# Performance work log

Measured on AMD Instinct MI355X. Metric: run time of the kernel, lower is better.

## Reference

```python
import jax, jax.numpy as jnp
import numpy as np

N_NODES = 100000
N_EDGES = 1600000
N_GRAPHS = 512
F_IN, HID, EMB = 256, 64, 2


def gcn_layer(h, src, dst, W, b, n_nodes):
    # PyG GCNConv: h' = D^{-1/2} (A + I) D^{-1/2} (h W) + b
    h = h @ W  # [N, out]
    loop = jnp.arange(n_nodes)
    s = jnp.concatenate([src, loop])
    d = jnp.concatenate([dst, loop])
    deg = jax.ops.segment_sum(jnp.ones_like(d, dtype=h.dtype), d, num_segments=n_nodes)
    dinv = jnp.where(deg > 0, jax.lax.rsqrt(deg), 0.0)
    norm = dinv[s] * dinv[d]  # [E+N]
    msg = h[s] * norm[:, None]  # gather + scale
    return jax.ops.segment_sum(msg, d, num_segments=n_nodes) + b


def setup_inputs() -> dict:
    key = jax.random.key(0)
    k1, k2, k3, k4, k5, k6 = jax.random.split(key, 6)
    x = jax.random.normal(k1, (N_NODES, F_IN), dtype=jnp.float32)
    edge_index = jax.random.randint(k2, (2, N_EDGES), 0, N_NODES, dtype=jnp.int64)
    batch = jnp.sort(jax.random.randint(k3, (N_NODES,), 0, N_GRAPHS, dtype=jnp.int64))
    # Glorot-ish init for layer weights
    W1 = jax.random.normal(k4, (F_IN, HID), dtype=jnp.float32) / np.sqrt(F_IN)
    b1 = jnp.zeros((HID,), dtype=jnp.float32)
    W2 = jax.random.normal(k5, (HID, EMB), dtype=jnp.float32) / np.sqrt(HID)
    b2 = jnp.zeros((EMB,), dtype=jnp.float32)
    return {"x": x, "edge_index": edge_index, "batch": batch,
            "W1": W1, "b1": b1, "W2": W2, "b2": b2}


def reference(x, edge_index, batch, W1, b1, W2, b2):
    n = x.shape[0]
    src, dst = edge_index[0], edge_index[1]
    h = gcn_layer(x, src, dst, W1, b1, n)
    h = jax.nn.relu(h)
    h = gcn_layer(h, src, dst, W2, b2, n)
    # global_mean_pool over graph ids
    sums = jax.ops.segment_sum(h, batch, num_segments=N_GRAPHS)
    cnts = jax.ops.segment_sum(jnp.ones((n,), dtype=h.dtype), batch, num_segments=N_GRAPHS)
    return sums / jnp.maximum(cnts, 1.0)[:, None]
```

## Files before the change

### kernel.cpp

```cpp
#include <hip/hip_runtime.h>
#include <hip/hip_bf16.h>

#define FIN 256
#define HID 64
#define EMB 2
#define BKB 9
#define BKSZ 512
#define MAXBK 256
#define NBLK 256
#define WPREP 8

typedef __bf16 bf16x8 __attribute__((ext_vector_type(8)));
typedef float  f32x16 __attribute__((ext_vector_type(16)));
typedef unsigned short u16x8 __attribute__((ext_vector_type(8)));

static __device__ __forceinline__ unsigned short f2bf(float f) {
    union { float f; unsigned int u; } v; v.f = f;
    unsigned int u = v.u;
    unsigned int r = (u + 0x7fffu + ((u >> 16) & 1u)) >> 16;
    return (unsigned short)r;
}
static __device__ __forceinline__ float bf2f(unsigned short h) {
    union { unsigned int u; float f; } v; v.u = ((unsigned int)h) << 16;
    return v.f;
}

__global__ __launch_bounds__(256) void bin_hist_kernel(
        const int* __restrict__ dst, int* __restrict__ counts,
        const float* __restrict__ W, __bf16* __restrict__ Bh, __bf16* __restrict__ Bl,
        int E, int chunk, int NBK) {
    if (blockIdx.x >= NBLK) {
        int t = (blockIdx.x - NBLK) * 256 + threadIdx.x;
        int ch = t >> 9, g = (t >> 6) & 7, m = t & 63;
        int kbase = ch * 64 + (g & 3) * 16 + ((m >> 5) << 3);
        int n = ((g >> 2) << 5) + (m & 31);
        bf16x8 hi, lo;
        #pragma unroll
        for (int q = 0; q < 8; ++q) {
            float w = W[(size_t)(kbase + q) * HID + n];
            __bf16 h = (__bf16)w;
            hi[q] = h; lo[q] = (__bf16)(w - (float)h);
        }
        *(bf16x8*)&Bh[(size_t)t * 8] = hi;
        *(bf16x8*)&Bl[(size_t)t * 8] = lo;
        return;
    }
    __shared__ int hist[MAXBK];
    int tid = threadIdx.x;
    for (int b = tid; b < NBK; b += 256) hist[b] = 0;
    __syncthreads();
    int e0 = blockIdx.x * chunk, e1 = min(e0 + chunk, E);
    if (e0 < e1) {
        const int4* d4 = (const int4*)(dst + e0);
        int nv = (e1 - e0) >> 2;
        for (int i = tid; i < nv; i += 256) {
            int4 v = d4[i];
            atomicAdd(&hist[v.x >> BKB], 1);
            atomicAdd(&hist[v.y >> BKB], 1);
            atomicAdd(&hist[v.z >> BKB], 1);
            atomicAdd(&hist[v.w >> BKB], 1);
        }
        for (int i = e0 + (nv << 2) + tid; i < e1; i += 256)
            atomicAdd(&hist[dst[i] >> BKB], 1);
    }
    __syncthreads();
    for (int b = tid; b < NBK; b += 256) counts[b * NBLK + blockIdx.x] = hist[b];
}

__global__ __launch_bounds__(256) void scan_local_kernel(
        int* __restrict__ counts, int* __restrict__ btot) {
    __shared__ int s[256];
    const int b = blockIdx.x, tid = threadIdx.x;
    int v = counts[b * NBLK + tid];
    s[tid] = v;
    __syncthreads();
    for (int off = 1; off < 256; off <<= 1) {
        int t = (tid >= off) ? s[tid - off] : 0;
        __syncthreads();
        s[tid] += t;
        __syncthreads();
    }
    counts[b * NBLK + tid] = s[tid] - v;
    if (tid == 255) btot[b] = s[255];
}

__global__ __launch_bounds__(256) void scan_tot_kernel(
        const int* __restrict__ btot, int* __restrict__ bucketBase,
        float* __restrict__ sums, int NBK, int nzero) {
    __shared__ int s[256];
    const int tid = threadIdx.x;
    int v = (tid < NBK) ? btot[tid] : 0;
    s[tid] = v;
    __syncthreads();
    for (int off = 1; off < 256; off <<= 1) {
        int t = (tid >= off) ? s[tid - off] : 0;
        __syncthreads();
        s[tid] += t;
        __syncthreads();
    }
    if (tid < NBK) bucketBase[tid] = s[tid] - v;
    if (tid == NBK - 1) bucketBase[NBK] = s[tid];
    for (int i = tid; i < nzero; i += 256) sums[i] = 0.f;
}

__global__ __launch_bounds__(256) void bin_scatter_kernel(
        const int* __restrict__ src, const int* __restrict__ dst,
        const int* __restrict__ counts, const int* __restrict__ bucketBase,
        unsigned* __restrict__ ebuf, int E, int chunk, int NBK) {
    __shared__ int cur[MAXBK];
    int tid = threadIdx.x;
    for (int b = tid; b < NBK; b += 256)
        cur[b] = bucketBase[b] + counts[b * NBLK + blockIdx.x];
    __syncthreads();
    int e0 = blockIdx.x * chunk, e1 = min(e0 + chunk, E);
    if (e0 >= e1) return;
    const int4* s4 = (const int4*)(src + e0);
    const int4* d4 = (const int4*)(dst + e0);
    int nv = (e1 - e0) >> 2;
    for (int i = tid; i < nv; i += 256) {
        int4 sv = s4[i], dv = d4[i];
        int b0 = dv.x >> BKB;
        int p0 = atomicAdd(&cur[b0], 1);
        ebuf[p0] = ((unsigned)sv.x << BKB) | (unsigned)(dv.x & (BKSZ - 1));
        int b1 = dv.y >> BKB;
        int p1 = atomicAdd(&cur[b1], 1);
        ebuf[p1] = ((unsigned)sv.y << BKB) | (unsigned)(dv.y & (BKSZ - 1));
        int b2 = dv.z >> BKB;
        int p2 = atomicAdd(&cur[b2], 1);
        ebuf[p2] = ((unsigned)sv.z << BKB) | (unsigned)(dv.z & (BKSZ - 1));
        int b3 = dv.w >> BKB;
        int p3 = atomicAdd(&cur[b3], 1);
        ebuf[p3] = ((unsigned)sv.w << BKB) | (unsigned)(dv.w & (BKSZ - 1));
    }
    for (int i = e0 + (nv << 2) + tid; i < e1; i += 256) {
        int s = src[i], d = dst[i];
        int b = d >> BKB;
        int pos = atomicAdd(&cur[b], 1);
        ebuf[pos] = ((unsigned)s << BKB) | (unsigned)(d & (BKSZ - 1));
    }
}

__global__ __launch_bounds__(256) void build_kernel(
        const unsigned* __restrict__ ebuf, const int* __restrict__ bucketBase,
        int* __restrict__ rowptr, float* __restrict__ dinv, int* __restrict__ csr,
        int N, int E) {
    __shared__ int hist[BKSZ];
    __shared__ int scanb[256];
    __shared__ int cur[BKSZ];
    const int b = blockIdx.x, tid = threadIdx.x;
    const int r0 = bucketBase[b];
    const int r1 = bucketBase[b + 1];
    const int nb0 = b * BKSZ;

    hist[tid] = 0; hist[tid + 256] = 0;
    __syncthreads();
    for (int i = r0 + tid; i < r1; i += 256)
        atomicAdd(&hist[ebuf[i] & (BKSZ - 1u)], 1);
    __syncthreads();

    int h0 = hist[2 * tid], h1 = hist[2 * tid + 1];
    if (nb0 + 2 * tid < N)     dinv[nb0 + 2 * tid]     = rsqrtf((float)h0 + 1.f);
    if (nb0 + 2 * tid + 1 < N) dinv[nb0 + 2 * tid + 1] = rsqrtf((float)h1 + 1.f);
    scanb[tid] = h0 + h1;
    __syncthreads();
    for (int off = 1; off < 256; off <<= 1) {
        int t = (tid >= off) ? scanb[tid - off] : 0;
        __syncthreads();
        scanb[tid] += t;
        __syncthreads();
    }
    int base0 = scanb[tid] - (h0 + h1);
    int o0 = base0, o1 = base0 + h0;
    cur[2 * tid] = o0; cur[2 * tid + 1] = o1;
    if (nb0 + 2 * tid < N)     rowptr[nb0 + 2 * tid]     = r0 + o0;
    if (nb0 + 2 * tid + 1 < N) rowptr[nb0 + 2 * tid + 1] = r0 + o1;
    if (nb0 + BKSZ >= N && tid == 0) rowptr[N] = E;
    __syncthreads();
    for (int i = r0 + tid; i < r1; i += 256) {
        unsigned u = ebuf[i];
        int loc = (int)(u & (BKSZ - 1u));
        int p = atomicAdd(&cur[loc], 1);
        csr[r0 + p] = (int)(u >> BKB);
    }
}

__global__ __launch_bounds__(256) void gemm1_kernel(
        const float* __restrict__ x,
        const __bf16* __restrict__ Bh, const __bf16* __restrict__ Bl,
        const float* __restrict__ dinv, unsigned short* __restrict__ h1b, int N) {
    __shared__ __align__(16) __bf16 A_hi[2 * 4 * 64 * 8];
    __shared__ __align__(16) __bf16 A_lo[2 * 4 * 64 * 8];

    const int tid = threadIdx.x;
    const int base = blockIdx.x * 64;
    const int w = tid >> 6;
    const int l = tid & 63;
    const int mg = w >> 1, ng = w & 1;

    const bf16x8* Bh8 = (const bf16x8*)Bh;
    const bf16x8* Bl8 = (const bf16x8*)Bl;

    f32x16 acc = {};

    const int r  = tid & 63;
    const int ks = tid >> 6;
    const int rl = r & 31, rh = r >> 5;

    for (int ch = 0; ch < 4; ++ch) {
        const int ck0 = ch * 64;
        __syncthreads();
        {
            int row = base + r;
            float f[16];
            if (row < N) {
                const float* xp = &x[(size_t)row * FIN + ck0 + ks * 16];
                float4 v0 = *(const float4*)(xp + 0);
                float4 v1 = *(const float4*)(xp + 4);
                float4 v2 = *(const float4*)(xp + 8);
                float4 v3 = *(const float4*)(xp + 12);
                f[0]=v0.x; f[1]=v0.y; f[2]=v0.z; f[3]=v0.w;
                f[4]=v1.x; f[5]=v1.y; f[6]=v1.z; f[7]=v1.w;
                f[8]=v2.x; f[9]=v2.y; f[10]=v2.z; f[11]=v2.w;
                f[12]=v3.x; f[13]=v3.y; f[14]=v3.z; f[15]=v3.w;
            } else {
                #pragma unroll
                for (int q = 0; q < 16; ++q) f[q] = 0.f;
            }
            bf16x8 ha, hb, la, lb;
            #pragma unroll
            for (int q = 0; q < 8; ++q) {
                __bf16 h0 = (__bf16)f[q];
                ha[q] = h0; la[q] = (__bf16)(f[q] - (float)h0);
                __bf16 h1v = (__bf16)f[q + 8];
                hb[q] = h1v; lb[q] = (__bf16)(f[q + 8] - (float)h1v);
            }
            int ra = ((rh * 4 + ks) * 64 + rl) * 8;
            int rb = ((rh * 4 + ks) * 64 + 32 + rl) * 8;
            *(bf16x8*)&A_hi[ra] = ha; *(bf16x8*)&A_hi[rb] = hb;
            *(bf16x8*)&A_lo[ra] = la; *(bf16x8*)&A_lo[rb] = lb;
        }
        __syncthreads();

        #pragma unroll
        for (int s = 0; s < 4; ++s) {
            bf16x8 a_h = *(const bf16x8*)&A_hi[((mg * 4 + s) * 64 + l) * 8];
            bf16x8 a_l = *(const bf16x8*)&A_lo[((mg * 4 + s) * 64 + l) * 8];
            int bv = (ch * 8 + ng * 4 + s) * 64 + l;
            bf16x8 b_h = Bh8[bv];
            bf16x8 b_l = Bl8[bv];
            acc = __builtin_amdgcn_mfma_f32_32x32x16_bf16(a_h, b_h, acc, 0, 0, 0);
            acc = __builtin_amdgcn_mfma_f32_32x32x16_bf16(a_h, b_l, acc, 0, 0, 0);
            acc = __builtin_amdgcn_mfma_f32_32x32x16_bf16(a_l, b_h, acc, 0, 0, 0);
        }
    }

    const int col = l & 31;
    const int rbase = 4 * (l >> 5);
    #pragma unroll
    for (int reg = 0; reg < 16; ++reg) {
        int row = (reg & 3) + 8 * (reg >> 2) + rbase;
        int node = base + mg * 32 + row;
        if (node < N)
            h1b[(size_t)node * HID + ng * 32 + col] = f2bf(acc[reg] * dinv[node]);
    }
}

__global__ __launch_bounds__(256) void agg1_layer2_kernel(
        const int* __restrict__ rowptr, const int* __restrict__ csr,
        const unsigned short* __restrict__ h1b,
        const float* __restrict__ dinv, const float* __restrict__ b1,
        const float* __restrict__ W2, float* __restrict__ h2, int N) {
    long t = (long)blockIdx.x * blockDim.x + threadIdx.x;
    int n = (int)(t >> 3);
    int li = threadIdx.x & 7;
    if (n >= N) return;
    const u16x8* h18 = (const u16x8*)h1b;

    float di = dinv[n];
    u16x8 sl = h18[(size_t)n * 8 + li];
    float v[8];
    #pragma unroll
    for (int k = 0; k < 8; ++k) v[k] = bf2f(sl[k]);

    int j0 = rowptr[n], j1 = rowptr[n + 1];
    int j = j0;
    for (; j + 7 < j1; j += 8) {
        int s0 = csr[j],     s1 = csr[j + 1], s2 = csr[j + 2], s3 = csr[j + 3];
        int s4 = csr[j + 4], s5 = csr[j + 5], s6 = csr[j + 6], s7 = csr[j + 7];
        u16x8 g0 = h18[(size_t)s0 * 8 + li];
        u16x8 g1 = h18[(size_t)s1 * 8 + li];
        u16x8 g2 = h18[(size_t)s2 * 8 + li];
        u16x8 g3 = h18[(size_t)s3 * 8 + li];
        u16x8 g4 = h18[(size_t)s4 * 8 + li];
        u16x8 g5 = h18[(size_t)s5 * 8 + li];
        u16x8 g6 = h18[(size_t)s6 * 8 + li];
        u16x8 g7 = h18[(size_t)s7 * 8 + li];
        #pragma unroll
        for (int k = 0; k < 8; ++k) {
            v[k] += bf2f(g0[k]) + bf2f(g1[k]) + bf2f(g2[k]) + bf2f(g3[k]);
            v[k] += bf2f(g4[k]) + bf2f(g5[k]) + bf2f(g6[k]) + bf2f(g7[k]);
        }
    }
    for (; j + 3 < j1; j += 4) {
        int s0 = csr[j], s1 = csr[j + 1], s2 = csr[j + 2], s3 = csr[j + 3];
        u16x8 g0 = h18[(size_t)s0 * 8 + li];
        u16x8 g1 = h18[(size_t)s1 * 8 + li];
        u16x8 g2 = h18[(size_t)s2 * 8 + li];
        u16x8 g3 = h18[(size_t)s3 * 8 + li];
        #pragma unroll
        for (int k = 0; k < 8; ++k)
            v[k] += bf2f(g0[k]) + bf2f(g1[k]) + bf2f(g2[k]) + bf2f(g3[k]);
    }
    for (; j < j1; ++j) {
        u16x8 g = h18[(size_t)csr[j] * 8 + li];
        #pragma unroll
        for (int k = 0; k < 8; ++k) v[k] += bf2f(g[k]);
    }

    const float4 ba = *(const float4*)&b1[li * 8];
    const float4 bb = *(const float4*)&b1[li * 8 + 4];
    v[0] = fmaxf(di * v[0] + ba.x, 0.f); v[1] = fmaxf(di * v[1] + ba.y, 0.f);
    v[2] = fmaxf(di * v[2] + ba.z, 0.f); v[3] = fmaxf(di * v[3] + ba.w, 0.f);
    v[4] = fmaxf(di * v[4] + bb.x, 0.f); v[5] = fmaxf(di * v[5] + bb.y, 0.f);
    v[6] = fmaxf(di * v[6] + bb.z, 0.f); v[7] = fmaxf(di * v[7] + bb.w, 0.f);

    const float4* W24 = (const float4*)W2;
    float r0 = 0.f, r1 = 0.f;
    #pragma unroll
    for (int k = 0; k < 4; ++k) {
        float4 wq = W24[li * 4 + k];
        r0 += v[2 * k] * wq.x + v[2 * k + 1] * wq.z;
        r1 += v[2 * k] * wq.y + v[2 * k + 1] * wq.w;
    }
    #pragma unroll
    for (int off = 1; off < 8; off <<= 1) {
        r0 += __shfl_xor(r0, off);
        r1 += __shfl_xor(r1, off);
    }
    if (li == 0) *(float2*)&h2[(size_t)n * EMB] = make_float2(r0 * di, r1 * di);
}

__global__ __launch_bounds__(256) void agg2_pool_kernel(
        const int* __restrict__ rowptr, const int* __restrict__ csr,
        const float* __restrict__ h2,
        const float* __restrict__ dinv, const float* __restrict__ b2,
        const int* __restrict__ batch,
        float* __restrict__ sums, float* __restrict__ cntf, int N) {
    int n = blockIdx.x * blockDim.x + threadIdx.x;
    int lane = threadIdx.x & 63;
    const float2* h2v = (const float2*)h2;
    float v0 = 0.f, v1 = 0.f, c = 0.f;
    int g = -1;
    if (n < N) {
        float di = dinv[n];
        float2 hs = h2v[n];
        v0 = hs.x; v1 = hs.y;
        int j0 = rowptr[n], j1 = rowptr[n + 1];
        int j = j0;
        for (; j + 7 < j1; j += 8) {
            int s0 = csr[j],     s1 = csr[j + 1], s2 = csr[j + 2], s3 = csr[j + 3];
            int s4 = csr[j + 4], s5 = csr[j + 5], s6 = csr[j + 6], s7 = csr[j + 7];
            float2 a = h2v[s0], b = h2v[s1], cc = h2v[s2], d = h2v[s3];
            float2 e = h2v[s4], f = h2v[s5], gg2 = h2v[s6], h = h2v[s7];
            v0 += a.x + b.x + cc.x + d.x;
            v1 += a.y + b.y + cc.y + d.y;
            v0 += e.x + f.x + gg2.x + h.x;
            v1 += e.y + f.y + gg2.y + h.y;
        }
        for (; j + 3 < j1; j += 4) {
            int s0 = csr[j], s1 = csr[j + 1], s2 = csr[j + 2], s3 = csr[j + 3];
            float2 a = h2v[s0], b = h2v[s1], cc = h2v[s2], d = h2v[s3];
            v0 += a.x + b.x + cc.x + d.x;
            v1 += a.y + b.y + cc.y + d.y;
        }
        for (; j < j1; ++j) {
            float2 hv = h2v[csr[j]];
            v0 += hv.x; v1 += hv.y;
        }
        v0 = di * v0 + b2[0];
        v1 = di * v1 + b2[1];
        g = batch[n];
        c = 1.f;
    }
    #pragma unroll
    for (int off = 1; off < 64; off <<= 1) {
        int gg = __shfl_up(g, off);
        float t0 = __shfl_up(v0, off);
        float t1 = __shfl_up(v1, off);
        float tc = __shfl_up(c, off);
        if (lane >= off && gg == g) { v0 += t0; v1 += t1; c += tc; }
    }
    int gn = __shfl_down(g, 1);
    if (g >= 0 && (lane == 63 || gn != g)) {
        atomicAdd(&sums[g * EMB + 0], v0);
        atomicAdd(&sums[g * EMB + 1], v1);
        atomicAdd(&cntf[g], c);
    }
}

__global__ void final_kernel(const float* __restrict__ sums, const float* __restrict__ cntf,
                             float* __restrict__ out, int G) {
    int g = blockIdx.x * blockDim.x + threadIdx.x;
    if (g >= G) return;
    float c = fmaxf(cntf[g], 1.0f);
    out[g * EMB + 0] = sums[g * EMB + 0] / c;
    out[g * EMB + 1] = sums[g * EMB + 1] / c;
}

extern "C" void kernel_launch(void* const* d_in, const int* in_sizes, int n_in,
                              void* d_out, int out_size, void* d_ws, size_t ws_size,
                              hipStream_t stream) {
    const float* x     = (const float*)d_in[0];
    const int*   ei    = (const int*)d_in[1];
    const int*   batch = (const int*)d_in[2];
    const float* W1    = (const float*)d_in[3];
    const float* b1    = (const float*)d_in[4];
    const float* W2    = (const float*)d_in[5];
    const float* b2    = (const float*)d_in[6];
    float* out = (float*)d_out;

    const int N = in_sizes[0] / FIN;
    const int E = in_sizes[1] / 2;
    const int G = out_size / EMB;
    const int* src = ei;
    const int* dst = ei + E;

    const int NBK = (N + BKSZ - 1) / BKSZ;
    const int chunk = (((E + NBLK - 1) / NBLK) + 3) & ~3;

    char* p = (char*)d_ws;
    auto take = [&](size_t bytes) { char* r = p; p += (bytes + 15) & ~(size_t)15; return r; };
    int*      counts = (int*)take(sizeof(int) * NBK * NBLK);
    int*      btot   = (int*)take(sizeof(int) * NBK);
    int*      bucketBase = (int*)take(sizeof(int) * (NBK + 1));
    unsigned* ebuf   = (unsigned*)take(sizeof(unsigned) * E);
    int*      csr    = (int*)take(sizeof(int) * E);
    int*      rowptr = (int*)take(sizeof(int) * (N + 1));
    float*    dinv   = (float*)take(sizeof(float) * N);
    unsigned short* h1b = (unsigned short*)take(sizeof(unsigned short) * (size_t)N * HID);
    float*    h2     = (float*)take(sizeof(float) * (size_t)N * EMB);
    float*    sums   = (float*)take(sizeof(float) * G * EMB);
    float*    cntf   = (float*)take(sizeof(float) * G);
    __bf16*   Bh     = (__bf16*)take(sizeof(__bf16) * 4 * 8 * 64 * 8);
    __bf16*   Bl     = (__bf16*)take(sizeof(__bf16) * 4 * 8 * 64 * 8);

    bin_hist_kernel<<<NBLK + WPREP, 256, 0, stream>>>(dst, counts, W1, Bh, Bl, E, chunk, NBK);
    scan_local_kernel<<<NBK, 256, 0, stream>>>(counts, btot);
    scan_tot_kernel<<<1, 256, 0, stream>>>(btot, bucketBase, sums, NBK, 3 * G);
    bin_scatter_kernel<<<NBLK, 256, 0, stream>>>(src, dst, counts, bucketBase, ebuf, E, chunk, NBK);
    build_kernel<<<NBK, 256, 0, stream>>>(ebuf, bucketBase, rowptr, dinv, csr, N, E);
    gemm1_kernel<<<(N + 63) / 64, 256, 0, stream>>>(x, Bh, Bl, dinv, h1b, N);
    agg1_layer2_kernel<<<(int)(((long)N * 8 + 255) / 256), 256, 0, stream>>>(
        rowptr, csr, h1b, dinv, b1, W2, h2, N);
    agg2_pool_kernel<<<(N + 255) / 256, 256, 0, stream>>>(
        rowptr, csr, h2, dinv, b2, batch, sums, cntf, N);
    final_kernel<<<(G + 255) / 256, 256, 0, stream>>>(sums, cntf, out, G);
}
```

Before: 288.8 us.

## Compute degrees early and overlap the layer-1 GEMM with CSR build kernels

Degrees are now counted with global atomics in the histogram pass, so dinv is ready before the CSR build. This lets the layer-1 GEMM tiles be split across the scan_tot, bin_scatter and build launches as extra blocks, running alongside the graph-preprocessing work instead of after it in a separate kernel. The cost is 1.6M extra global atomics on the degree array, a new prep kernel to zero it, and GEMM blocks competing for CU resources and shared memory with the binning blocks.

```diff
diff --git a/kernel.cpp b/kernel.cpp
--- a/kernel.cpp
+++ b/kernel.cpp
@@ -25,174 +25,15 @@
     return v.f;
 }
 
-__global__ __launch_bounds__(256) void bin_hist_kernel(
-        const int* __restrict__ dst, int* __restrict__ counts,
-        const float* __restrict__ W, __bf16* __restrict__ Bh, __bf16* __restrict__ Bl,
-        int E, int chunk, int NBK) {
-    if (blockIdx.x >= NBLK) {
-        int t = (blockIdx.x - NBLK) * 256 + threadIdx.x;
-        int ch = t >> 9, g = (t >> 6) & 7, m = t & 63;
-        int kbase = ch * 64 + (g & 3) * 16 + ((m >> 5) << 3);
-        int n = ((g >> 2) << 5) + (m & 31);
-        bf16x8 hi, lo;
-        #pragma unroll
-        for (int q = 0; q < 8; ++q) {
-            float w = W[(size_t)(kbase + q) * HID + n];
-            __bf16 h = (__bf16)w;
-            hi[q] = h; lo[q] = (__bf16)(w - (float)h);
-        }
-        *(bf16x8*)&Bh[(size_t)t * 8] = hi;
-        *(bf16x8*)&Bl[(size_t)t * 8] = lo;
-        return;
-    }
-    __shared__ int hist[MAXBK];
-    int tid = threadIdx.x;
-    for (int b = tid; b < NBK; b += 256) hist[b] = 0;
-    __syncthreads();
-    int e0 = blockIdx.x * chunk, e1 = min(e0 + chunk, E);
-    if (e0 < e1) {
-        const int4* d4 = (const int4*)(dst + e0);
-        int nv = (e1 - e0) >> 2;
-        for (int i = tid; i < nv; i += 256) {
-            int4 v = d4[i];
-            atomicAdd(&hist[v.x >> BKB], 1);
-            atomicAdd(&hist[v.y >> BKB], 1);
-            atomicAdd(&hist[v.z >> BKB], 1);
-            atomicAdd(&hist[v.w >> BKB], 1);
-        }
-        for (int i = e0 + (nv << 2) + tid; i < e1; i += 256)
-            atomicAdd(&hist[dst[i] >> BKB], 1);
-    }
-    __syncthreads();
-    for (int b = tid; b < NBK; b += 256) counts[b * NBLK + blockIdx.x] = hist[b];
-}
-
-__global__ __launch_bounds__(256) void scan_local_kernel(
-        int* __restrict__ counts, int* __restrict__ btot) {
-    __shared__ int s[256];
-    const int b = blockIdx.x, tid = threadIdx.x;
-    int v = counts[b * NBLK + tid];
-    s[tid] = v;
-    __syncthreads();
-    for (int off = 1; off < 256; off <<= 1) {
-        int t = (tid >= off) ? s[tid - off] : 0;
-        __syncthreads();
-        s[tid] += t;
-        __syncthreads();
-    }
-    counts[b * NBLK + tid] = s[tid] - v;
-    if (tid == 255) btot[b] = s[255];
-}
-
-__global__ __launch_bounds__(256) void scan_tot_kernel(
-        const int* __restrict__ btot, int* __restrict__ bucketBase,
-        float* __restrict__ sums, int NBK, int nzero) {
-    __shared__ int s[256];
-    const int tid = threadIdx.x;
-    int v = (tid < NBK) ? btot[tid] : 0;
-    s[tid] = v;
-    __syncthreads();
-    for (int off = 1; off < 256; off <<= 1) {
-        int t = (tid >= off) ? s[tid - off] : 0;
-        __syncthreads();
-        s[tid] += t;
-        __syncthreads();
-    }
-    if (tid < NBK) bucketBase[tid] = s[tid] - v;
-    if (tid == NBK - 1) bucketBase[NBK] = s[tid];
-    for (int i = tid; i < nzero; i += 256) sums[i] = 0.f;
-}
-
-__global__ __launch_bounds__(256) void bin_scatter_kernel(
-        const int* __restrict__ src, const int* __restrict__ dst,
-        const int* __restrict__ counts, const int* __restrict__ bucketBase,
-        unsigned* __restrict__ ebuf, int E, int chunk, int NBK) {
-    __shared__ int cur[MAXBK];
-    int tid = threadIdx.x;
-    for (int b = tid; b < NBK; b += 256)
-        cur[b] = bucketBase[b] + counts[b * NBLK + blockIdx.x];
-    __syncthreads();
-    int e0 = blockIdx.x * chunk, e1 = min(e0 + chunk, E);
-    if (e0 >= e1) return;
-    const int4* s4 = (const int4*)(src + e0);
-    const int4* d4 = (const int4*)(dst + e0);
-    int nv = (e1 - e0) >> 2;
-    for (int i = tid; i < nv; i += 256) {
-        int4 sv = s4[i], dv = d4[i];
-        int b0 = dv.x >> BKB;
-        int p0 = atomicAdd(&cur[b0], 1);
-        ebuf[p0] = ((unsigned)sv.x << BKB) | (unsigned)(dv.x & (BKSZ - 1));
-        int b1 = dv.y >> BKB;
-        int p1 = atomicAdd(&cur[b1], 1);
-        ebuf[p1] = ((unsigned)sv.y << BKB) | (unsigned)(dv.y & (BKSZ - 1));
-        int b2 = dv.z >> BKB;
-        int p2 = atomicAdd(&cur[b2], 1);
-        ebuf[p2] = ((unsigned)sv.z << BKB) | (unsigned)(dv.z & (BKSZ - 1));
-        int b3 = dv.w >> BKB;
-        int p3 = atomicAdd(&cur[b3], 1);
-        ebuf[p3] = ((unsigned)sv.w << BKB) | (unsigned)(dv.w & (BKSZ - 1));
-    }
-    for (int i = e0 + (nv << 2) + tid; i < e1; i += 256) {
-        int s = src[i], d = dst[i];
-        int b = d >> BKB;
-        int pos = atomicAdd(&cur[b], 1);
-        ebuf[pos] = ((unsigned)s << BKB) | (unsigned)(d & (BKSZ - 1));
-    }
-}
-
-__global__ __launch_bounds__(256) void build_kernel(
-        const unsigned* __restrict__ ebuf, const int* __restrict__ bucketBase,
-        int* __restrict__ rowptr, float* __restrict__ dinv, int* __restrict__ csr,
-        int N, int E) {
-    __shared__ int hist[BKSZ];
-    __shared__ int scanb[256];
-    __shared__ int cur[BKSZ];
-    const int b = blockIdx.x, tid = threadIdx.x;
-    const int r0 = bucketBase[b];
-    const int r1 = bucketBase[b + 1];
-    const int nb0 = b * BKSZ;
-
-    hist[tid] = 0; hist[tid + 256] = 0;
-    __syncthreads();
-    for (int i = r0 + tid; i < r1; i += 256)
-        atomicAdd(&hist[ebuf[i] & (BKSZ - 1u)], 1);
-    __syncthreads();
-
-    int h0 = hist[2 * tid], h1 = hist[2 * tid + 1];
-    if (nb0 + 2 * tid < N)     dinv[nb0 + 2 * tid]     = rsqrtf((float)h0 + 1.f);
-    if (nb0 + 2 * tid + 1 < N) dinv[nb0 + 2 * tid + 1] = rsqrtf((float)h1 + 1.f);
-    scanb[tid] = h0 + h1;
-    __syncthreads();
-    for (int off = 1; off < 256; off <<= 1) {
-        int t = (tid >= off) ? scanb[tid - off] : 0;
-        __syncthreads();
-        scanb[tid] += t;
-        __syncthreads();
-    }
-    int base0 = scanb[tid] - (h0 + h1);
-    int o0 = base0, o1 = base0 + h0;
-    cur[2 * tid] = o0; cur[2 * tid + 1] = o1;
-    if (nb0 + 2 * tid < N)     rowptr[nb0 + 2 * tid]     = r0 + o0;
-    if (nb0 + 2 * tid + 1 < N) rowptr[nb0 + 2 * tid + 1] = r0 + o1;
-    if (nb0 + BKSZ >= N && tid == 0) rowptr[N] = E;
-    __syncthreads();
-    for (int i = r0 + tid; i < r1; i += 256) {
-        unsigned u = ebuf[i];
-        int loc = (int)(u & (BKSZ - 1u));
-        int p = atomicAdd(&cur[loc], 1);
-        csr[r0 + p] = (int)(u >> BKB);
-    }
-}
-
-__global__ __launch_bounds__(256) void gemm1_kernel(
-        const float* __restrict__ x,
+static __device__ void gemm_tile(
+        int gb, const float* __restrict__ x,
         const __bf16* __restrict__ Bh, const __bf16* __restrict__ Bl,
         const float* __restrict__ dinv, unsigned short* __restrict__ h1b, int N) {
     __shared__ __align__(16) __bf16 A_hi[2 * 4 * 64 * 8];
     __shared__ __align__(16) __bf16 A_lo[2 * 4 * 64 * 8];
 
     const int tid = threadIdx.x;
-    const int base = blockIdx.x * 64;
+    const int base = gb * 64;
     const int w = tid >> 6;
     const int l = tid & 63;
     const int mg = w >> 1, ng = w & 1;
@@ -265,6 +106,206 @@
     }
 }
 
+__global__ __launch_bounds__(256) void prep_kernel(
+        const float* __restrict__ W, __bf16* __restrict__ Bh, __bf16* __restrict__ Bl,
+        int* __restrict__ deg, float* __restrict__ sums, int N, int nzero) {
+    if (blockIdx.x < WPREP) {
+        int t = blockIdx.x * 256 + threadIdx.x;
+        int ch = t >> 9, g = (t >> 6) & 7, m = t & 63;
+        int kbase = ch * 64 + (g & 3) * 16 + ((m >> 5) << 3);
+        int n = ((g >> 2) << 5) + (m & 31);
+        bf16x8 hi, lo;
+        #pragma unroll
+        for (int q = 0; q < 8; ++q) {
+            float w = W[(size_t)(kbase + q) * HID + n];
+            __bf16 h = (__bf16)w;
+            hi[q] = h; lo[q] = (__bf16)(w - (float)h);
+        }
+        *(bf16x8*)&Bh[(size_t)t * 8] = hi;
+        *(bf16x8*)&Bl[(size_t)t * 8] = lo;
+        return;
+    }
+    int t = (blockIdx.x - WPREP) * 256 + threadIdx.x;
+    int stride = (gridDim.x - WPREP) * 256;
+    for (int i = t; i < N; i += stride) deg[i] = 0;
+    for (int i = t; i < nzero; i += stride) sums[i] = 0.f;
+}
+
+__global__ __launch_bounds__(256) void bin_hist_kernel(
+        const int* __restrict__ dst, int* __restrict__ counts, int* __restrict__ deg,
+        int E, int chunk, int NBK) {
+    __shared__ int hist[MAXBK];
+    int tid = threadIdx.x;
+    for (int b = tid; b < NBK; b += 256) hist[b] = 0;
+    __syncthreads();
+    int e0 = blockIdx.x * chunk, e1 = min(e0 + chunk, E);
+    if (e0 < e1) {
+        const int4* d4 = (const int4*)(dst + e0);
+        int nv = (e1 - e0) >> 2;
+        for (int i = tid; i < nv; i += 256) {
+            int4 v = d4[i];
+            atomicAdd(&hist[v.x >> BKB], 1);
+            atomicAdd(&hist[v.y >> BKB], 1);
+            atomicAdd(&hist[v.z >> BKB], 1);
+            atomicAdd(&hist[v.w >> BKB], 1);
+            atomicAdd(&deg[v.x], 1);
+            atomicAdd(&deg[v.y], 1);
+            atomicAdd(&deg[v.z], 1);
+            atomicAdd(&deg[v.w], 1);
+        }
+        for (int i = e0 + (nv << 2) + tid; i < e1; i += 256) {
+            int d = dst[i];
+            atomicAdd(&hist[d >> BKB], 1);
+            atomicAdd(&deg[d], 1);
+        }
+    }
+    __syncthreads();
+    for (int b = tid; b < NBK; b += 256) counts[b * NBLK + blockIdx.x] = hist[b];
+}
+
+__global__ __launch_bounds__(256) void scan_local_kernel(
+        int* __restrict__ counts, int* __restrict__ btot,
+        const int* __restrict__ deg, float* __restrict__ dinv, int NBK, int N) {
+    __shared__ int s[256];
+    const int tid = threadIdx.x;
+    if (blockIdx.x >= NBK) {
+        int n0 = (blockIdx.x - NBK) * BKSZ;
+        int n1 = min(n0 + BKSZ, N);
+        for (int i = n0 + tid; i < n1; i += 256)
+            dinv[i] = rsqrtf((float)deg[i] + 1.f);
+        return;
+    }
+    const int b = blockIdx.x;
+    int v = counts[b * NBLK + tid];
+    s[tid] = v;
+    __syncthreads();
+    for (int off = 1; off < 256; off <<= 1) {
+        int t = (tid >= off) ? s[tid - off] : 0;
+        __syncthreads();
+        s[tid] += t;
+        __syncthreads();
+    }
+    counts[b * NBLK + tid] = s[tid] - v;
+    if (tid == 255) btot[b] = s[255];
+}
+
+__global__ __launch_bounds__(256) void scan_tot_kernel(
+        const int* __restrict__ btot, int* __restrict__ bucketBase, int NBK,
+        const float* __restrict__ x, const __bf16* __restrict__ Bh,
+        const __bf16* __restrict__ Bl, const float* __restrict__ dinv,
+        unsigned short* __restrict__ h1b, int N) {
+    if (blockIdx.x > 0) {
+        gemm_tile(blockIdx.x - 1, x, Bh, Bl, dinv, h1b, N);
+        return;
+    }
+    __shared__ int s[256];
+    const int tid = threadIdx.x;
+    int v = (tid < NBK) ? btot[tid] : 0;
+    s[tid] = v;
+    __syncthreads();
+    for (int off = 1; off < 256; off <<= 1) {
+        int t = (tid >= off) ? s[tid - off] : 0;
+        __syncthreads();
+        s[tid] += t;
+        __syncthreads();
+    }
+    if (tid < NBK) bucketBase[tid] = s[tid] - v;
+    if (tid == NBK - 1) bucketBase[NBK] = s[tid];
+}
+
+__global__ __launch_bounds__(256) void bin_scatter_kernel(
+        const int* __restrict__ src, const int* __restrict__ dst,
+        const int* __restrict__ counts, const int* __restrict__ bucketBase,
+        unsigned* __restrict__ ebuf, int E, int chunk, int NBK,
+        const float* __restrict__ x, const __bf16* __restrict__ Bh,
+        const __bf16* __restrict__ Bl, const float* __restrict__ dinv,
+        unsigned short* __restrict__ h1b, int N, int g0) {
+    if (blockIdx.x >= NBLK) {
+        gemm_tile(g0 + (int)blockIdx.x - NBLK, x, Bh, Bl, dinv, h1b, N);
+        return;
+    }
+    __shared__ int cur[MAXBK];
+    int tid = threadIdx.x;
+    for (int b = tid; b < NBK; b += 256)
+        cur[b] = bucketBase[b] + counts[b * NBLK + blockIdx.x];
+    __syncthreads();
+    int e0 = blockIdx.x * chunk, e1 = min(e0 + chunk, E);
+    if (e0 >= e1) return;
+    const int4* s4 = (const int4*)(src + e0);
+    const int4* d4 = (const int4*)(dst + e0);
+    int nv = (e1 - e0) >> 2;
+    for (int i = tid; i < nv; i += 256) {
+        int4 sv = s4[i], dv = d4[i];
+        int b0 = dv.x >> BKB;
+        int p0 = atomicAdd(&cur[b0], 1);
+        ebuf[p0] = ((unsigned)sv.x << BKB) | (unsigned)(dv.x & (BKSZ - 1));
+        int b1 = dv.y >> BKB;
+        int p1 = atomicAdd(&cur[b1], 1);
+        ebuf[p1] = ((unsigned)sv.y << BKB) | (unsigned)(dv.y & (BKSZ - 1));
+        int b2 = dv.z >> BKB;
+        int p2 = atomicAdd(&cur[b2], 1);
+        ebuf[p2] = ((unsigned)sv.z << BKB) | (unsigned)(dv.z & (BKSZ - 1));
+        int b3 = dv.w >> BKB;
+        int p3 = atomicAdd(&cur[b3], 1);
+        ebuf[p3] = ((unsigned)sv.w << BKB) | (unsigned)(dv.w & (BKSZ - 1));
+    }
+    for (int i = e0 + (nv << 2) + tid; i < e1; i += 256) {
+        int s = src[i], d = dst[i];
+        int b = d >> BKB;
+        int pos = atomicAdd(&cur[b], 1);
+        ebuf[pos] = ((unsigned)s << BKB) | (unsigned)(d & (BKSZ - 1));
+    }
+}
+
+__global__ __launch_bounds__(256) void build_kernel(
+        const unsigned* __restrict__ ebuf, const int* __restrict__ bucketBase,
+        int* __restrict__ rowptr, int* __restrict__ csr, int N, int E,
+        const float* __restrict__ x, const __bf16* __restrict__ Bh,
+        const __bf16* __restrict__ Bl, const float* __restrict__ dinv,
+        unsigned short* __restrict__ h1b, int g0) {
+    const int NBK = (N + BKSZ - 1) >> BKB;
+    if ((int)blockIdx.x >= NBK) {
+        gemm_tile(g0 + (int)blockIdx.x - NBK, x, Bh, Bl, dinv, h1b, N);
+        return;
+    }
+    __shared__ int hist[BKSZ];
+    __shared__ int scanb[256];
+    __shared__ int cur[BKSZ];
+    const int b = blockIdx.x, tid = threadIdx.x;
+    const int r0 = bucketBase[b];
+    const int r1 = bucketBase[b + 1];
+    const int nb0 = b * BKSZ;
+
+    hist[tid] = 0; hist[tid + 256] = 0;
+    __syncthreads();
+    for (int i = r0 + tid; i < r1; i += 256)
+        atomicAdd(&hist[ebuf[i] & (BKSZ - 1u)], 1);
+    __syncthreads();
+
+    int h0 = hist[2 * tid], h1 = hist[2 * tid + 1];
+    scanb[tid] = h0 + h1;
+    __syncthreads();
+    for (int off = 1; off < 256; off <<= 1) {
+        int t = (tid >= off) ? scanb[tid - off] : 0;
+        __syncthreads();
+        scanb[tid] += t;
+        __syncthreads();
+    }
+    int base0 = scanb[tid] - (h0 + h1);
+    int o0 = base0, o1 = base0 + h0;
+    cur[2 * tid] = o0; cur[2 * tid + 1] = o1;
+    if (nb0 + 2 * tid < N)     rowptr[nb0 + 2 * tid]     = r0 + o0;
+    if (nb0 + 2 * tid + 1 < N) rowptr[nb0 + 2 * tid + 1] = r0 + o1;
+    if (nb0 + BKSZ >= N && tid == 0) rowptr[N] = E;
+    __syncthreads();
+    for (int i = r0 + tid; i < r1; i += 256) {
+        unsigned u = ebuf[i];
+        int loc = (int)(u & (BKSZ - 1u));
+        int p = atomicAdd(&cur[loc], 1);
+        csr[r0 + p] = (int)(u >> BKB);
+    }
+}
+
 __global__ __launch_bounds__(256) void agg1_layer2_kernel(
         const int* __restrict__ rowptr, const int* __restrict__ csr,
         const unsigned short* __restrict__ h1b,
@@ -437,6 +478,7 @@
     int*      csr    = (int*)take(sizeof(int) * E);
     int*      rowptr = (int*)take(sizeof(int) * (N + 1));
     float*    dinv   = (float*)take(sizeof(float) * N);
+    int*      deg    = (int*)take(sizeof(int) * N);
     unsigned short* h1b = (unsigned short*)take(sizeof(unsigned short) * (size_t)N * HID);
     float*    h2     = (float*)take(sizeof(float) * (size_t)N * EMB);
     float*    sums   = (float*)take(sizeof(float) * G * EMB);
@@ -444,12 +486,23 @@
     __bf16*   Bh     = (__bf16*)take(sizeof(__bf16) * 4 * 8 * 64 * 8);
     __bf16*   Bl     = (__bf16*)take(sizeof(__bf16) * 4 * 8 * 64 * 8);
 
-    bin_hist_kernel<<<NBLK + WPREP, 256, 0, stream>>>(dst, counts, W1, Bh, Bl, E, chunk, NBK);
-    scan_local_kernel<<<NBK, 256, 0, stream>>>(counts, btot);
-    scan_tot_kernel<<<1, 256, 0, stream>>>(btot, bucketBase, sums, NBK, 3 * G);
-    bin_scatter_kernel<<<NBLK, 256, 0, stream>>>(src, dst, counts, bucketBase, ebuf, E, chunk, NBK);
-    build_kernel<<<NBK, 256, 0, stream>>>(ebuf, bucketBase, rowptr, dinv, csr, N, E);
-    gemm1_kernel<<<(N + 63) / 64, 256, 0, stream>>>(x, Bh, Bl, dinv, h1b, N);
+    const int T  = (N + 63) / 64;
+    const int s3 = (T < 400) ? T : 400;
+    const int s4 = (T - s3 < 600) ? (T - s3) : 600;
+    const int s5 = T - s3 - s4;
+
+    prep_kernel<<<WPREP + 128, 256, 0, stream>>>(W1, Bh, Bl, deg, sums, N, 3 * G);
+    bin_hist_kernel<<<NBLK, 256, 0, stream>>>(dst, counts, deg, E, chunk, NBK);
+    scan_local_kernel<<<NBK + (N + BKSZ - 1) / BKSZ, 256, 0, stream>>>(
+        counts, btot, deg, dinv, NBK, N);
+    scan_tot_kernel<<<1 + s3, 256, 0, stream>>>(btot, bucketBase, NBK,
+                                                x, Bh, Bl, dinv, h1b, N);
+    bin_scatter_kernel<<<NBLK + s4, 256, 0, stream>>>(
+        src, dst, counts, bucketBase, ebuf, E, chunk, NBK,
+        x, Bh, Bl, dinv, h1b, N, s3);
+    build_kernel<<<NBK + s5, 256, 0, stream>>>(
+        ebuf, bucketBase, rowptr, csr, N, E,
+        x, Bh, Bl, dinv, h1b, s3 + s4);
     agg1_layer2_kernel<<<(int)(((long)N * 8 + 255) / 256), 256, 0, stream>>>(
         rowptr, csr, h1b, dinv, b1, W2, h2, N);
     agg2_pool_kernel<<<(N + 255) / 256, 256, 0, stream>>>(
```

New measurement: 349.6 us. 21.1% more time.

## Fuse CSR build chain into one cooperative kernel and fold final into pool

Applied to the files above, without the earlier changes.

Replaces the five preprocessing kernels (histogram, two scans, scatter, bucket build) with a single cooperative kernel of 512 blocks that uses grid-wide syncs between phases. The bucket-total scan is recomputed redundantly per block. The final mean division is folded into the pooling kernel through a last-block-done counter. The aim is to remove kernel launch gaps and tail idle time across many small dependent stages, at the cost of grid.sync overhead and redundant scans.

```diff
diff --git a/kernel.cpp b/kernel.cpp
--- a/kernel.cpp
+++ b/kernel.cpp
@@ -1,13 +1,13 @@
 #include <hip/hip_runtime.h>
 #include <hip/hip_bf16.h>
+#include <hip/hip_cooperative_groups.h>
 
 #define FIN 256
 #define HID 64
 #define EMB 2
 #define BKB 9
 #define BKSZ 512
-#define MAXBK 256
-#define NBLK 256
+#define CGRID 512
 #define WPREP 8
 
 typedef __bf16 bf16x8 __attribute__((ext_vector_type(8)));
@@ -25,162 +25,177 @@
     return v.f;
 }
 
-__global__ __launch_bounds__(256) void bin_hist_kernel(
-        const int* __restrict__ dst, int* __restrict__ counts,
-        const float* __restrict__ W, __bf16* __restrict__ Bh, __bf16* __restrict__ Bl,
-        int E, int chunk, int NBK) {
-    if (blockIdx.x >= NBLK) {
-        int t = (blockIdx.x - NBLK) * 256 + threadIdx.x;
+struct CoopArgs {
+    const int* src; const int* dst;
+    int* counts; int* btot;
+    unsigned* ebuf; int* csr; int* rowptr; float* dinv;
+    const float* W1; __bf16* Bh; __bf16* Bl;
+    float* pool;
+    int E, chunk, NBK, N, G;
+};
+
+__global__ __launch_bounds__(256, 2) void coop_chain_kernel(CoopArgs a) {
+    namespace cg = cooperative_groups;
+    cg::grid_group grid = cg::this_grid();
+    __shared__ int hist[BKSZ];
+    __shared__ int scanb[256];
+    __shared__ int cur[BKSZ];
+
+    const int bi  = blockIdx.x;
+    const int tid = threadIdx.x;
+    const int NBK = a.NBK;
+
+    for (int b = tid; b < NBK; b += 256) hist[b] = 0;
+    __syncthreads();
+    {
+        int e0 = bi * a.chunk, e1 = min(e0 + a.chunk, a.E);
+        if (e0 < e1) {
+            const int4* d4 = (const int4*)(a.dst + e0);
+            int nv = (e1 - e0) >> 2;
+            for (int i = tid; i < nv; i += 256) {
+                int4 v = d4[i];
+                atomicAdd(&hist[v.x >> BKB], 1);
+                atomicAdd(&hist[v.y >> BKB], 1);
+                atomicAdd(&hist[v.z >> BKB], 1);
+                atomicAdd(&hist[v.w >> BKB], 1);
+            }
+            for (int i = e0 + (nv << 2) + tid; i < e1; i += 256)
+                atomicAdd(&hist[a.dst[i] >> BKB], 1);
+        }
+    }
+    __syncthreads();
+    for (int b = tid; b < NBK; b += 256) a.counts[b * CGRID + bi] = hist[b];
+    __threadfence();
+    grid.sync();
+
+    if (bi < NBK) {
+        int c0 = a.counts[bi * CGRID + 2 * tid];
+        int c1 = a.counts[bi * CGRID + 2 * tid + 1];
+        int pair = c0 + c1;
+        scanb[tid] = pair;
+        __syncthreads();
+        for (int off = 1; off < 256; off <<= 1) {
+            int t = (tid >= off) ? scanb[tid - off] : 0;
+            __syncthreads();
+            scanb[tid] += t;
+            __syncthreads();
+        }
+        int base = scanb[tid] - pair;
+        a.counts[bi * CGRID + 2 * tid]     = base;
+        a.counts[bi * CGRID + 2 * tid + 1] = base + c0;
+        if (tid == 255) a.btot[bi] = scanb[255];
+    } else if (bi < NBK + WPREP) {
+        int t = (bi - NBK) * 256 + tid;
         int ch = t >> 9, g = (t >> 6) & 7, m = t & 63;
         int kbase = ch * 64 + (g & 3) * 16 + ((m >> 5) << 3);
         int n = ((g >> 2) << 5) + (m & 31);
         bf16x8 hi, lo;
         #pragma unroll
         for (int q = 0; q < 8; ++q) {
-            float w = W[(size_t)(kbase + q) * HID + n];
+            float w = a.W1[(size_t)(kbase + q) * HID + n];
             __bf16 h = (__bf16)w;
             hi[q] = h; lo[q] = (__bf16)(w - (float)h);
         }
-        *(bf16x8*)&Bh[(size_t)t * 8] = hi;
-        *(bf16x8*)&Bl[(size_t)t * 8] = lo;
-        return;
-    }
-    __shared__ int hist[MAXBK];
-    int tid = threadIdx.x;
-    for (int b = tid; b < NBK; b += 256) hist[b] = 0;
-    __syncthreads();
-    int e0 = blockIdx.x * chunk, e1 = min(e0 + chunk, E);
-    if (e0 < e1) {
-        const int4* d4 = (const int4*)(dst + e0);
-        int nv = (e1 - e0) >> 2;
-        for (int i = tid; i < nv; i += 256) {
-            int4 v = d4[i];
-            atomicAdd(&hist[v.x >> BKB], 1);
-            atomicAdd(&hist[v.y >> BKB], 1);
-            atomicAdd(&hist[v.z >> BKB], 1);
-            atomicAdd(&hist[v.w >> BKB], 1);
-        }
-        for (int i = e0 + (nv << 2) + tid; i < e1; i += 256)
-            atomicAdd(&hist[dst[i] >> BKB], 1);
-    }
-    __syncthreads();
-    for (int b = tid; b < NBK; b += 256) counts[b * NBLK + blockIdx.x] = hist[b];
-}
-
-__global__ __launch_bounds__(256) void scan_local_kernel(
-        int* __restrict__ counts, int* __restrict__ btot) {
-    __shared__ int s[256];
-    const int b = blockIdx.x, tid = threadIdx.x;
-    int v = counts[b * NBLK + tid];
-    s[tid] = v;
-    __syncthreads();
-    for (int off = 1; off < 256; off <<= 1) {
-        int t = (tid >= off) ? s[tid - off] : 0;
-        __syncthreads();
-        s[tid] += t;
-        __syncthreads();
-    }
-    counts[b * NBLK + tid] = s[tid] - v;
-    if (tid == 255) btot[b] = s[255];
-}
-
-__global__ __launch_bounds__(256) void scan_tot_kernel(
-        const int* __restrict__ btot, int* __restrict__ bucketBase,
-        float* __restrict__ sums, int NBK, int nzero) {
-    __shared__ int s[256];
-    const int tid = threadIdx.x;
-    int v = (tid < NBK) ? btot[tid] : 0;
-    s[tid] = v;
-    __syncthreads();
-    for (int off = 1; off < 256; off <<= 1) {
-        int t = (tid >= off) ? s[tid - off] : 0;
-        __syncthreads();
-        s[tid] += t;
-        __syncthreads();
-    }
-    if (tid < NBK) bucketBase[tid] = s[tid] - v;
-    if (tid == NBK - 1) bucketBase[NBK] = s[tid];
-    for (int i = tid; i < nzero; i += 256) sums[i] = 0.f;
-}
-
-__global__ __launch_bounds__(256) void bin_scatter_kernel(
-        const int* __restrict__ src, const int* __restrict__ dst,
-        const int* __restrict__ counts, const int* __restrict__ bucketBase,
-        unsigned* __restrict__ ebuf, int E, int chunk, int NBK) {
-    __shared__ int cur[MAXBK];
-    int tid = threadIdx.x;
-    for (int b = tid; b < NBK; b += 256)
-        cur[b] = bucketBase[b] + counts[b * NBLK + blockIdx.x];
-    __syncthreads();
-    int e0 = blockIdx.x * chunk, e1 = min(e0 + chunk, E);
-    if (e0 >= e1) return;
-    const int4* s4 = (const int4*)(src + e0);
-    const int4* d4 = (const int4*)(dst + e0);
-    int nv = (e1 - e0) >> 2;
-    for (int i = tid; i < nv; i += 256) {
-        int4 sv = s4[i], dv = d4[i];
-        int b0 = dv.x >> BKB;
-        int p0 = atomicAdd(&cur[b0], 1);
-        ebuf[p0] = ((unsigned)sv.x << BKB) | (unsigned)(dv.x & (BKSZ - 1));
-        int b1 = dv.y >> BKB;
-        int p1 = atomicAdd(&cur[b1], 1);
-        ebuf[p1] = ((unsigned)sv.y << BKB) | (unsigned)(dv.y & (BKSZ - 1));
-        int b2 = dv.z >> BKB;
-        int p2 = atomicAdd(&cur[b2], 1);
-        ebuf[p2] = ((unsigned)sv.z << BKB) | (unsigned)(dv.z & (BKSZ - 1));
-        int b3 = dv.w >> BKB;
-        int p3 = atomicAdd(&cur[b3], 1);
-        ebuf[p3] = ((unsigned)sv.w << BKB) | (unsigned)(dv.w & (BKSZ - 1));
-    }
-    for (int i = e0 + (nv << 2) + tid; i < e1; i += 256) {
-        int s = src[i], d = dst[i];
-        int b = d >> BKB;
-        int pos = atomicAdd(&cur[b], 1);
-        ebuf[pos] = ((unsigned)s << BKB) | (unsigned)(d & (BKSZ - 1));
-    }
-}
-
-__global__ __launch_bounds__(256) void build_kernel(
-        const unsigned* __restrict__ ebuf, const int* __restrict__ bucketBase,
-        int* __restrict__ rowptr, float* __restrict__ dinv, int* __restrict__ csr,
-        int N, int E) {
-    __shared__ int hist[BKSZ];
-    __shared__ int scanb[256];
-    __shared__ int cur[BKSZ];
-    const int b = blockIdx.x, tid = threadIdx.x;
-    const int r0 = bucketBase[b];
-    const int r1 = bucketBase[b + 1];
-    const int nb0 = b * BKSZ;
-
-    hist[tid] = 0; hist[tid + 256] = 0;
-    __syncthreads();
-    for (int i = r0 + tid; i < r1; i += 256)
-        atomicAdd(&hist[ebuf[i] & (BKSZ - 1u)], 1);
-    __syncthreads();
-
-    int h0 = hist[2 * tid], h1 = hist[2 * tid + 1];
-    if (nb0 + 2 * tid < N)     dinv[nb0 + 2 * tid]     = rsqrtf((float)h0 + 1.f);
-    if (nb0 + 2 * tid + 1 < N) dinv[nb0 + 2 * tid + 1] = rsqrtf((float)h1 + 1.f);
-    scanb[tid] = h0 + h1;
-    __syncthreads();
-    for (int off = 1; off < 256; off <<= 1) {
-        int t = (tid >= off) ? scanb[tid - off] : 0;
-        __syncthreads();
-        scanb[tid] += t;
-        __syncthreads();
-    }
-    int base0 = scanb[tid] - (h0 + h1);
-    int o0 = base0, o1 = base0 + h0;
-    cur[2 * tid] = o0; cur[2 * tid + 1] = o1;
-    if (nb0 + 2 * tid < N)     rowptr[nb0 + 2 * tid]     = r0 + o0;
-    if (nb0 + 2 * tid + 1 < N) rowptr[nb0 + 2 * tid + 1] = r0 + o1;
-    if (nb0 + BKSZ >= N && tid == 0) rowptr[N] = E;
-    __syncthreads();
-    for (int i = r0 + tid; i < r1; i += 256) {
-        unsigned u = ebuf[i];
-        int loc = (int)(u & (BKSZ - 1u));
-        int p = atomicAdd(&cur[loc], 1);
-        csr[r0 + p] = (int)(u >> BKB);
+        *(bf16x8*)&a.Bh[(size_t)t * 8] = hi;
+        *(bf16x8*)&a.Bl[(size_t)t * 8] = lo;
+    } else if (bi == NBK + WPREP) {
+        for (int i = tid; i < 3 * a.G + 1; i += 256) a.pool[i] = 0.f;
+    }
+    __threadfence();
+    grid.sync();
+
+    {
+        int v = (tid < NBK) ? a.btot[tid] : 0;
+        scanb[tid] = v;
+        __syncthreads();
+        for (int off = 1; off < 256; off <<= 1) {
+            int t = (tid >= off) ? scanb[tid - off] : 0;
+            __syncthreads();
+            scanb[tid] += t;
+            __syncthreads();
+        }
+        if (tid < NBK) hist[tid] = scanb[tid] - v;
+        __syncthreads();
+        for (int b = tid; b < NBK; b += 256)
+            cur[b] = hist[b] + a.counts[b * CGRID + bi];
+        __syncthreads();
+
+        int e0 = bi * a.chunk, e1 = min(e0 + a.chunk, a.E);
+        if (e0 < e1) {
+            const int4* s4 = (const int4*)(a.src + e0);
+            const int4* d4 = (const int4*)(a.dst + e0);
+            int nv = (e1 - e0) >> 2;
+            for (int i = tid; i < nv; i += 256) {
+                int4 sv = s4[i], dv = d4[i];
+                int b0 = dv.x >> BKB;
+                int p0 = atomicAdd(&cur[b0], 1);
+                a.ebuf[p0] = ((unsigned)sv.x << BKB) | (unsigned)(dv.x & (BKSZ - 1));
+                int b1 = dv.y >> BKB;
+                int p1 = atomicAdd(&cur[b1], 1);
+                a.ebuf[p1] = ((unsigned)sv.y << BKB) | (unsigned)(dv.y & (BKSZ - 1));
+                int b2 = dv.z >> BKB;
+                int p2 = atomicAdd(&cur[b2], 1);
+                a.ebuf[p2] = ((unsigned)sv.z << BKB) | (unsigned)(dv.z & (BKSZ - 1));
+                int b3 = dv.w >> BKB;
+                int p3 = atomicAdd(&cur[b3], 1);
+                a.ebuf[p3] = ((unsigned)sv.w << BKB) | (unsigned)(dv.w & (BKSZ - 1));
+            }
+            for (int i = e0 + (nv << 2) + tid; i < e1; i += 256) {
+                int s = a.src[i], d = a.dst[i];
+                int b = d >> BKB;
+                int pos = atomicAdd(&cur[b], 1);
+                a.ebuf[pos] = ((unsigned)s << BKB) | (unsigned)(d & (BKSZ - 1));
+            }
+        }
+    }
+    __threadfence();
+    grid.sync();
+
+    if (bi < NBK) {
+        int v = (tid < NBK) ? a.btot[tid] : 0;
+        scanb[tid] = v;
+        __syncthreads();
+        for (int off = 1; off < 256; off <<= 1) {
+            int t = (tid >= off) ? scanb[tid - off] : 0;
+            __syncthreads();
+            scanb[tid] += t;
+            __syncthreads();
+        }
+        const int r1 = scanb[bi];
+        const int r0 = r1 - a.btot[bi];
+        const int nb0 = bi * BKSZ;
+        __syncthreads();
+
+        hist[tid] = 0; hist[tid + 256] = 0;
+        __syncthreads();
+        for (int i = r0 + tid; i < r1; i += 256)
+            atomicAdd(&hist[a.ebuf[i] & (BKSZ - 1u)], 1);
+        __syncthreads();
+
+        int h0 = hist[2 * tid], h1 = hist[2 * tid + 1];
+        if (nb0 + 2 * tid < a.N)     a.dinv[nb0 + 2 * tid]     = rsqrtf((float)h0 + 1.f);
+        if (nb0 + 2 * tid + 1 < a.N) a.dinv[nb0 + 2 * tid + 1] = rsqrtf((float)h1 + 1.f);
+        scanb[tid] = h0 + h1;
+        __syncthreads();
+        for (int off = 1; off < 256; off <<= 1) {
+            int t = (tid >= off) ? scanb[tid - off] : 0;
+            __syncthreads();
+            scanb[tid] += t;
+            __syncthreads();
+        }
+        int base0 = scanb[tid] - (h0 + h1);
+        int o0 = base0, o1 = base0 + h0;
+        cur[2 * tid] = o0; cur[2 * tid + 1] = o1;
+        if (nb0 + 2 * tid < a.N)     a.rowptr[nb0 + 2 * tid]     = r0 + o0;
+        if (nb0 + 2 * tid + 1 < a.N) a.rowptr[nb0 + 2 * tid + 1] = r0 + o1;
+        if (nb0 + BKSZ >= a.N && tid == 0) a.rowptr[a.N] = a.E;
+        __syncthreads();
+        for (int i = r0 + tid; i < r1; i += 256) {
+            unsigned u = a.ebuf[i];
+            int loc = (int)(u & (BKSZ - 1u));
+            int p = atomicAdd(&cur[loc], 1);
+            a.csr[r0 + p] = (int)(u >> BKB);
+        }
     }
 }
 
@@ -340,12 +355,13 @@
     if (li == 0) *(float2*)&h2[(size_t)n * EMB] = make_float2(r0 * di, r1 * di);
 }
 
-__global__ __launch_bounds__(256) void agg2_pool_kernel(
+__global__ __launch_bounds__(256) void agg2_pool_final_kernel(
         const int* __restrict__ rowptr, const int* __restrict__ csr,
         const float* __restrict__ h2,
         const float* __restrict__ dinv, const float* __restrict__ b2,
         const int* __restrict__ batch,
-        float* __restrict__ sums, float* __restrict__ cntf, int N) {
+        float* __restrict__ sums, float* __restrict__ cntf, int* __restrict__ done,
+        float* __restrict__ out, int N, int G) {
     int n = blockIdx.x * blockDim.x + threadIdx.x;
     int lane = threadIdx.x & 63;
     const float2* h2v = (const float2*)h2;
@@ -396,15 +412,20 @@
         atomicAdd(&sums[g * EMB + 1], v1);
         atomicAdd(&cntf[g], c);
     }
-}
-
-__global__ void final_kernel(const float* __restrict__ sums, const float* __restrict__ cntf,
-                             float* __restrict__ out, int G) {
-    int g = blockIdx.x * blockDim.x + threadIdx.x;
-    if (g >= G) return;
-    float c = fmaxf(cntf[g], 1.0f);
-    out[g * EMB + 0] = sums[g * EMB + 0] / c;
-    out[g * EMB + 1] = sums[g * EMB + 1] / c;
+
+    __shared__ int sdone;
+    __threadfence();
+    if (threadIdx.x == 0) sdone = atomicAdd(done, 1);
+    __syncthreads();
+    if (sdone == (int)gridDim.x - 1) {
+        for (int i = threadIdx.x; i < G; i += 256) {
+            float s0 = atomicAdd(&sums[i * EMB + 0], 0.f);
+            float s1 = atomicAdd(&sums[i * EMB + 1], 0.f);
+            float cc = fmaxf(atomicAdd(&cntf[i], 0.f), 1.0f);
+            out[i * EMB + 0] = s0 / cc;
+            out[i * EMB + 1] = s1 / cc;
+        }
+    }
 }
 
 extern "C" void kernel_launch(void* const* d_in, const int* in_sizes, int n_in,
@@ -426,33 +447,36 @@
     const int* dst = ei + E;
 
     const int NBK = (N + BKSZ - 1) / BKSZ;
-    const int chunk = (((E + NBLK - 1) / NBLK) + 3) & ~3;
+    const int chunk = (((E + CGRID - 1) / CGRID) + 3) & ~3;
 
     char* p = (char*)d_ws;
     auto take = [&](size_t bytes) { char* r = p; p += (bytes + 15) & ~(size_t)15; return r; };
-    int*      counts = (int*)take(sizeof(int) * NBK * NBLK);
+    int*      counts = (int*)take(sizeof(int) * NBK * CGRID);
     int*      btot   = (int*)take(sizeof(int) * NBK);
-    int*      bucketBase = (int*)take(sizeof(int) * (NBK + 1));
     unsigned* ebuf   = (unsigned*)take(sizeof(unsigned) * E);
     int*      csr    = (int*)take(sizeof(int) * E);
     int*      rowptr = (int*)take(sizeof(int) * (N + 1));
     float*    dinv   = (float*)take(sizeof(float) * N);
     unsigned short* h1b = (unsigned short*)take(sizeof(unsigned short) * (size_t)N * HID);
     float*    h2     = (float*)take(sizeof(float) * (size_t)N * EMB);
-    float*    sums   = (float*)take(sizeof(float) * G * EMB);
-    float*    cntf   = (float*)take(sizeof(float) * G);
+    float*    pool   = (float*)take(sizeof(float) * (3 * G + 4));
     __bf16*   Bh     = (__bf16*)take(sizeof(__bf16) * 4 * 8 * 64 * 8);
     __bf16*   Bl     = (__bf16*)take(sizeof(__bf16) * 4 * 8 * 64 * 8);
-
-    bin_hist_kernel<<<NBLK + WPREP, 256, 0, stream>>>(dst, counts, W1, Bh, Bl, E, chunk, NBK);
-    scan_local_kernel<<<NBK, 256, 0, stream>>>(counts, btot);
-    scan_tot_kernel<<<1, 256, 0, stream>>>(btot, bucketBase, sums, NBK, 3 * G);
-    bin_scatter_kernel<<<NBLK, 256, 0, stream>>>(src, dst, counts, bucketBase, ebuf, E, chunk, NBK);
-    build_kernel<<<NBK, 256, 0, stream>>>(ebuf, bucketBase, rowptr, dinv, csr, N, E);
+    float*    sums   = pool;
+    float*    cntf   = pool + 2 * G;
+    int*      done   = (int*)(pool + 3 * G);
+
+    CoopArgs ca;
+    ca.src = src; ca.dst = dst; ca.counts = counts; ca.btot = btot;
+    ca.ebuf = ebuf; ca.csr = csr; ca.rowptr = rowptr; ca.dinv = dinv;
+    ca.W1 = W1; ca.Bh = Bh; ca.Bl = Bl; ca.pool = pool;
+    ca.E = E; ca.chunk = chunk; ca.NBK = NBK; ca.N = N; ca.G = G;
+    void* kargs[] = { (void*)&ca };
+    hipLaunchCooperativeKernel((void*)coop_chain_kernel, dim3(CGRID), dim3(256),
+                               kargs, 0, stream);
     gemm1_kernel<<<(N + 63) / 64, 256, 0, stream>>>(x, Bh, Bl, dinv, h1b, N);
     agg1_layer2_kernel<<<(int)(((long)N * 8 + 255) / 256), 256, 0, stream>>>(
         rowptr, csr, h1b, dinv, b1, W2, h2, N);
-    agg2_pool_kernel<<<(N + 255) / 256, 256, 0, stream>>>(
-        rowptr, csr, h2, dinv, b2, batch, sums, cntf, N);
-    final_kernel<<<(G + 255) / 256, 256, 0, stream>>>(sums, cntf, out, G);
-}
+    agg2_pool_final_kernel<<<(N + 255) / 256, 256, 0, stream>>>(
+        rowptr, csr, h2, dinv, b2, batch, sums, cntf, done, out, N, G);
+}
```

Result: slower. 674.0 us (+133.4%).
